# Kernel tuning notes

Measured on AMD Instinct MI355X. Metric: run time of the kernel, lower is better.

The kernel has to match this reference:

```python
import jax, jax.numpy as jnp
import numpy as np

B, N, M, G, F = 8, 1000, 64, 50, 128


def setup_inputs() -> dict:
    key = jax.random.key(0)
    ks = jax.random.split(key, 9)
    s = 0.05
    return {
        "features": jax.random.normal(ks[0], (B, N, F), jnp.float32),
        "rbf_expansion": jax.random.uniform(ks[1], (B, N, M, G), jnp.float32),
        "neighbor_list": jax.random.randint(ks[2], (B, N, M), 0, N, jnp.int64),
        "W_init": jax.random.normal(ks[3], (F, F), jnp.float32) * s,
        "W1": jax.random.normal(ks[4], (G, F), jnp.float32) * s,
        "b1": jnp.zeros((F,), jnp.float32),
        "W2": jax.random.normal(ks[5], (F, F), jnp.float32) * s,
        "b2": jnp.zeros((F,), jnp.float32),
        "nbr_w": jax.random.normal(ks[6], (F,), jnp.float32) * s,
        "Wo1": jax.random.normal(ks[7], (F, F), jnp.float32) * s,
        "bo1": jnp.zeros((F,), jnp.float32),
        "Wo2": jax.random.normal(ks[8], (F, F), jnp.float32) * s,
        "bo2": jnp.zeros((F,), jnp.float32),
    }


def reference(features, rbf_expansion, neighbor_list, W_init, W1, b1, W2, b2,
              nbr_w, Wo1, bo1, Wo2, bo2):
    b, n, m = neighbor_list.shape
    # 1. atom-wise linear, no bias/activation: [B,N,F]
    init = features @ W_init
    # 2. CFConv: filter generator on RBF expansion -> [B,N,M,F]
    filt = jnp.tanh(rbf_expansion @ W1 + b1) @ W2 + b2
    # gather neighbor features: init[b, neighbor_list[b,n,m], :] -> [B,N,M,F]
    idx = neighbor_list.reshape(b, n * m, 1)
    nbr_feat = jnp.take_along_axis(init, idx, axis=1).reshape(b, n, m, -1)
    conv = nbr_feat * filt
    # attention over neighbors via learned vector nbr_w
    attn = jax.nn.softmax(jnp.einsum('bnmf,f->bnm', conv, nbr_w), axis=-1)
    agg = jnp.einsum('bnm,bnmf->bnf', attn, conv)
    # 3-4. output dense: linear+tanh, then linear
    out = jnp.tanh(agg @ Wo1 + bo1) @ Wo2 + bo2
    return out, attn
```

## Files before the change

### kernel.cpp

```cpp
#include <hip/hip_runtime.h>
#include <hip/hip_bf16.h>

typedef __attribute__((ext_vector_type(8))) short short8;
typedef __attribute__((ext_vector_type(4))) float f32x4;
typedef unsigned short u16;
typedef unsigned int u32;

#define NBATCH 8
#define NA 1000
#define MD 64
#define GD 50
#define FD 128
#define TOTAL (NBATCH * NA)

__device__ __forceinline__ u16 f2bf(float f) {
    u32 x = __float_as_uint(f);
    return (u16)((x + 0x7fffu + ((x >> 16) & 1u)) >> 16);
}
__device__ __forceinline__ float bf2f(u16 u) {
    return __uint_as_float(((u32)u) << 16);
}
__device__ __forceinline__ u32 pkbf(float x, float y) {
    __hip_bfloat162 h = __float22bfloat162_rn(float2{x, y});
    return *reinterpret_cast<u32*>(&h);
}
__device__ __forceinline__ float tanh_fast(float x) {
    float e = __expf(2.0f * x);
    return 1.0f - 2.0f * __builtin_amdgcn_rcpf(e + 1.0f);
}
__device__ __forceinline__ f32x4 mfma16(short8 a, short8 b, f32x4 c) {
    return __builtin_amdgcn_mfma_f32_16x16x32_bf16(a, b, c, 0, 0, 0);
}

__global__ void k0_prep(const float* __restrict__ W1, const float* __restrict__ W2,
                        const float* __restrict__ Wi, const float* __restrict__ Wo1,
                        const float* __restrict__ Wo2,
                        u16* __restrict__ W1T, u16* __restrict__ W2T,
                        u16* __restrict__ WiT, u16* __restrict__ Wo1T,
                        u16* __restrict__ Wo2T) {
    const int g0 = blockIdx.x * 256 + threadIdx.x;
    const int gstep = gridDim.x * 256;
    for (int i = g0; i < 128 * 72; i += gstep) {
        int n = i / 72, k = i - n * 72;
        int ks = (k < GD) ? k : 0;
        W1T[i] = (k < GD) ? f2bf(W1[ks * FD + n]) : (u16)0;
    }
    for (int i = g0; i < 2 * 128 * 72; i += gstep) {
        int p = i / 9216;
        int rem = i - p * 9216;
        int n = rem / 72, kk = rem - n * 72;
        bool valid = kk < 64;
        int k = p * 64 + (valid ? kk : 0);
        W2T[i]  = valid ? f2bf(W2[k * FD + n])  : (u16)0;
        WiT[i]  = valid ? f2bf(Wi[k * FD + n])  : (u16)0;
        Wo1T[i] = valid ? f2bf(Wo1[k * FD + n]) : (u16)0;
        Wo2T[i] = valid ? f2bf(Wo2[k * FD + n]) : (u16)0;
    }
}

__global__ __launch_bounds__(256, 3) void k1_init(const float* __restrict__ feat,
                                                  const u16* __restrict__ WiT,
                                                  u16* __restrict__ initB) {
    __shared__ alignas(16) char smem[53248];
    u16* sA = (u16*)smem;
    u16* sW = (u16*)(smem + 34816);
    const int tid = threadIdx.x, wid = tid >> 6, lane = tid & 63;
    const int quad = lane >> 4, col = lane & 15, rw = wid * 32;
    const int row0 = blockIdx.x * 128;

    for (int i = tid; i < 4096; i += 256) {
        int r = i >> 5, c = (i & 31) * 4;
        int gr = row0 + r;
        float4 v = {0.f, 0.f, 0.f, 0.f};
        if (gr < TOTAL) v = *(const float4*)&feat[(size_t)gr * FD + c];
        u32* p = (u32*)&sA[r * 136 + c];
        p[0] = pkbf(v.x, v.y);
        p[1] = pkbf(v.z, v.w);
    }
    for (int i = tid; i < 1152; i += 256) ((int4*)sW)[i] = ((const int4*)WiT)[i];
    __syncthreads();

    f32x4 acc[2][8];
    const f32x4 zf = {0.f, 0.f, 0.f, 0.f};
#pragma unroll
    for (int mt = 0; mt < 2; ++mt)
#pragma unroll
        for (int nt = 0; nt < 8; ++nt) acc[mt][nt] = zf;

    for (int half = 0; half < 2; ++half) {
        if (half) {
            __syncthreads();
            for (int i = tid; i < 1152; i += 256)
                ((int4*)sW)[i] = ((const int4*)(WiT + 9216))[i];
            __syncthreads();
        }
#pragma unroll
        for (int ks = 0; ks < 2; ++ks) {
            const int ka = half * 64 + ks * 32 + quad * 8;
            const int kb = ks * 32 + quad * 8;
            short8 a0 = *(const short8*)&sA[(rw + col) * 136 + ka];
            short8 a1 = *(const short8*)&sA[(rw + 16 + col) * 136 + ka];
#pragma unroll
            for (int nt = 0; nt < 8; ++nt) {
                short8 bfr = *(const short8*)&sW[(nt * 16 + col) * 72 + kb];
                acc[0][nt] = mfma16(a0, bfr, acc[0][nt]);
                acc[1][nt] = mfma16(a1, bfr, acc[1][nt]);
            }
        }
    }
#pragma unroll
    for (int mt = 0; mt < 2; ++mt)
#pragma unroll
        for (int nt = 0; nt < 8; ++nt)
#pragma unroll
            for (int r = 0; r < 4; ++r) {
                int row = rw + mt * 16 + quad * 4 + r;
                int gr = row0 + row;
                if (gr < TOTAL)
                    initB[(size_t)gr * FD + nt * 16 + col] = f2bf(acc[mt][nt][r]);
            }
}

__global__ __launch_bounds__(256, 3) void k2_main(
    const float* __restrict__ rbf, const int* __restrict__ nl,
    const u16* __restrict__ initB,
    const u16* __restrict__ W1T, const u16* __restrict__ W2T,
    const float* __restrict__ b1, const float* __restrict__ b2,
    const float* __restrict__ nbrw,
    float* __restrict__ aggOut, float* __restrict__ attnO) {
    __shared__ alignas(16) char smem[53760];
    u16* sA = (u16*)smem;
    u16* sB = (u16*)(smem + 34816);
    int* nlS = (int*)(smem + 53248);
    float* logitS = (float*)smem;
    float* attnS  = (float*)(smem + 512);
    float* aggS   = (float*)(smem + 1024);

    const int tid = threadIdx.x, wid = tid >> 6, lane = tid & 63;
    const int quad = lane >> 4, col = lane & 15, rw = wid * 32;
    const int blk = blockIdx.x;
    const int b = blk / 500;
    const int n0 = (blk - b * 500) * 2;
    const int atom0 = b * NA + n0;
    const size_t rbf_base = (size_t)atom0 * (MD * GD);

    if (tid < 128) nlS[tid] = nl[atom0 * MD + tid];
    for (int i = tid; i < 128 * 14; i += 256) {
        int r = i / 14;
        sA[r * 72 + 50 + (i - r * 14)] = 0;
    }
    for (int i = tid; i < 3200; i += 256) {
        int e = 2 * i;
        int r = e / 50, g = e - r * 50;
        float2 v = *(const float2*)&rbf[rbf_base + e];
        *(u32*)&sA[r * 72 + g] = pkbf(v.x, v.y);
    }
    for (int i = tid; i < 1152; i += 256) ((int4*)sB)[i] = ((const int4*)W1T)[i];
    __syncthreads();

    f32x4 acc[2][8];
    const f32x4 zf = {0.f, 0.f, 0.f, 0.f};
#pragma unroll
    for (int mt = 0; mt < 2; ++mt)
#pragma unroll
        for (int nt = 0; nt < 8; ++nt) acc[mt][nt] = zf;
#pragma unroll
    for (int ks = 0; ks < 2; ++ks) {
        const int ka = ks * 32 + quad * 8;
        short8 a0 = *(const short8*)&sA[(rw + col) * 72 + ka];
        short8 a1 = *(const short8*)&sA[(rw + 16 + col) * 72 + ka];
#pragma unroll
        for (int nt = 0; nt < 8; ++nt) {
            short8 bfr = *(const short8*)&sB[(nt * 16 + col) * 72 + ka];
            acc[0][nt] = mfma16(a0, bfr, acc[0][nt]);
            acc[1][nt] = mfma16(a1, bfr, acc[1][nt]);
        }
    }
    __syncthreads();

    float bias[8];
#pragma unroll
    for (int nt = 0; nt < 8; ++nt) bias[nt] = b1[nt * 16 + col];
#pragma unroll
    for (int mt = 0; mt < 2; ++mt)
#pragma unroll
        for (int nt = 0; nt < 8; ++nt)
#pragma unroll
            for (int r = 0; r < 4; ++r) {
                int row = rw + mt * 16 + quad * 4 + r;
                sA[row * 136 + nt * 16 + col] =
                    f2bf(tanh_fast(acc[mt][nt][r] + bias[nt]));
            }
    for (int i = tid; i < 1152; i += 256) ((int4*)sB)[i] = ((const int4*)W2T)[i];
    __syncthreads();

    f32x4 acc2[2][8];
#pragma unroll
    for (int mt = 0; mt < 2; ++mt)
#pragma unroll
        for (int nt = 0; nt < 8; ++nt) acc2[mt][nt] = zf;
    for (int half = 0; half < 2; ++half) {
        if (half) {
            __syncthreads();
            for (int i = tid; i < 1152; i += 256)
                ((int4*)sB)[i] = ((const int4*)(W2T + 9216))[i];
            __syncthreads();
        }
#pragma unroll
        for (int ks = 0; ks < 2; ++ks) {
            const int ka = half * 64 + ks * 32 + quad * 8;
            const int kb = ks * 32 + quad * 8;
            short8 a0 = *(const short8*)&sA[(rw + col) * 136 + ka];
            short8 a1 = *(const short8*)&sA[(rw + 16 + col) * 136 + ka];
#pragma unroll
            for (int nt = 0; nt < 8; ++nt) {
                short8 bfr = *(const short8*)&sB[(nt * 16 + col) * 72 + kb];
                acc2[0][nt] = mfma16(a0, bfr, acc2[0][nt]);
                acc2[1][nt] = mfma16(a1, bfr, acc2[1][nt]);
            }
        }
    }

    float wv[8];
#pragma unroll
    for (int nt = 0; nt < 8; ++nt) {
        bias[nt] = b2[nt * 16 + col];
        wv[nt] = nbrw[nt * 16 + col];
    }
    int rowoff[2][4];
#pragma unroll
    for (int mt = 0; mt < 2; ++mt)
#pragma unroll
        for (int r = 0; r < 4; ++r) {
            int rr = rw + mt * 16 + quad * 4 + r;
            rowoff[mt][r] = (b * NA + nlS[rr]) * FD;
        }
    float part[2][4] = {{0.f, 0.f, 0.f, 0.f}, {0.f, 0.f, 0.f, 0.f}};
#pragma unroll
    for (int mt = 0; mt < 2; ++mt)
#pragma unroll
        for (int nt = 0; nt < 8; ++nt)
#pragma unroll
            for (int r = 0; r < 4; ++r) {
                float nb = bf2f(initB[rowoff[mt][r] + nt * 16 + col]);
                float cv = nb * (acc2[mt][nt][r] + bias[nt]);
                acc2[mt][nt][r] = cv;
                part[mt][r] += cv * wv[nt];
            }
#pragma unroll
    for (int d = 1; d < 16; d <<= 1)
#pragma unroll
        for (int mt = 0; mt < 2; ++mt)
#pragma unroll
            for (int r = 0; r < 4; ++r)
                part[mt][r] += __shfl_xor(part[mt][r], d, 64);
    __syncthreads();
    if (col == 0) {
#pragma unroll
        for (int mt = 0; mt < 2; ++mt)
#pragma unroll
            for (int r = 0; r < 4; ++r)
                logitS[rw + mt * 16 + quad * 4 + r] = part[mt][r];
    }
    __syncthreads();

    if (wid < 2) {
        float x = logitS[wid * 64 + lane];
        float m = x;
#pragma unroll
        for (int d = 1; d < 64; d <<= 1) m = fmaxf(m, __shfl_xor(m, d, 64));
        float e = __expf(x - m);
        float s = e;
#pragma unroll
        for (int d = 1; d < 64; d <<= 1) s += __shfl_xor(s, d, 64);
        float a = e / s;
        attnS[wid * 64 + lane] = a;
        attnO[(size_t)(atom0 + wid) * MD + lane] = a;
    }
    __syncthreads();

    float aggp[8] = {0.f, 0.f, 0.f, 0.f, 0.f, 0.f, 0.f, 0.f};
#pragma unroll
    for (int mt = 0; mt < 2; ++mt)
#pragma unroll
        for (int r = 0; r < 4; ++r) {
            float a = attnS[rw + mt * 16 + quad * 4 + r];
#pragma unroll
            for (int nt = 0; nt < 8; ++nt) aggp[nt] += a * acc2[mt][nt][r];
        }
#pragma unroll
    for (int d = 16; d < 64; d <<= 1)
#pragma unroll
        for (int nt = 0; nt < 8; ++nt) aggp[nt] += __shfl_xor(aggp[nt], d, 64);
    if (quad == 0) {
#pragma unroll
        for (int nt = 0; nt < 8; ++nt) aggS[wid * 128 + nt * 16 + col] = aggp[nt];
    }
    __syncthreads();
    {
        int a = tid >> 7;
        int c = tid & 127;
        float v = aggS[(2 * a) * 128 + c] + aggS[(2 * a + 1) * 128 + c];
        aggOut[(size_t)(atom0 + a) * FD + c] = v;
    }
}

__global__ __launch_bounds__(256, 3) void k3_out(
    float* __restrict__ outp, const u16* __restrict__ Wo1T,
    const u16* __restrict__ Wo2T, const float* __restrict__ bo1,
    const float* __restrict__ bo2) {
    __shared__ alignas(16) char smem[53248];
    u16* sA = (u16*)smem;
    u16* sW = (u16*)(smem + 34816);
    const int tid = threadIdx.x, wid = tid >> 6, lane = tid & 63;
    const int quad = lane >> 4, col = lane & 15, rw = wid * 32;
    const int row0 = blockIdx.x * 128;

    for (int i = tid; i < 4096; i += 256) {
        int r = i >> 5, c = (i & 31) * 4;
        int gr = row0 + r;
        float4 v = {0.f, 0.f, 0.f, 0.f};
        if (gr < TOTAL) v = *(const float4*)&outp[(size_t)gr * FD + c];
        u32* p = (u32*)&sA[r * 136 + c];
        p[0] = pkbf(v.x, v.y);
        p[1] = pkbf(v.z, v.w);
    }
    for (int i = tid; i < 1152; i += 256) ((int4*)sW)[i] = ((const int4*)Wo1T)[i];
    __syncthreads();

    f32x4 acc[2][8];
    const f32x4 zf = {0.f, 0.f, 0.f, 0.f};
#pragma unroll
    for (int mt = 0; mt < 2; ++mt)
#pragma unroll
        for (int nt = 0; nt < 8; ++nt) acc[mt][nt] = zf;
    for (int half = 0; half < 2; ++half) {
        if (half) {
            __syncthreads();
            for (int i = tid; i < 1152; i += 256)
                ((int4*)sW)[i] = ((const int4*)(Wo1T + 9216))[i];
            __syncthreads();
        }
#pragma unroll
        for (int ks = 0; ks < 2; ++ks) {
            const int ka = half * 64 + ks * 32 + quad * 8;
            const int kb = ks * 32 + quad * 8;
            short8 a0 = *(const short8*)&sA[(rw + col) * 136 + ka];
            short8 a1 = *(const short8*)&sA[(rw + 16 + col) * 136 + ka];
#pragma unroll
            for (int nt = 0; nt < 8; ++nt) {
                short8 bfr = *(const short8*)&sW[(nt * 16 + col) * 72 + kb];
                acc[0][nt] = mfma16(a0, bfr, acc[0][nt]);
                acc[1][nt] = mfma16(a1, bfr, acc[1][nt]);
            }
        }
    }
    __syncthreads();

    float bias[8];
#pragma unroll
    for (int nt = 0; nt < 8; ++nt) bias[nt] = bo1[nt * 16 + col];
#pragma unroll
    for (int mt = 0; mt < 2; ++mt)
#pragma unroll
        for (int nt = 0; nt < 8; ++nt)
#pragma unroll
            for (int r = 0; r < 4; ++r) {
                int row = rw + mt * 16 + quad * 4 + r;
                sA[row * 136 + nt * 16 + col] =
                    f2bf(tanh_fast(acc[mt][nt][r] + bias[nt]));
            }
    for (int i = tid; i < 1152; i += 256) ((int4*)sW)[i] = ((const int4*)Wo2T)[i];
    __syncthreads();

    f32x4 acc2[2][8];
#pragma unroll
    for (int mt = 0; mt < 2; ++mt)
#pragma unroll
        for (int nt = 0; nt < 8; ++nt) acc2[mt][nt] = zf;
    for (int half = 0; half < 2; ++half) {
        if (half) {
            __syncthreads();
            for (int i = tid; i < 1152; i += 256)
                ((int4*)sW)[i] = ((const int4*)(Wo2T + 9216))[i];
            __syncthreads();
        }
#pragma unroll
        for (int ks = 0; ks < 2; ++ks) {
            const int ka = half * 64 + ks * 32 + quad * 8;
            const int kb = ks * 32 + quad * 8;
            short8 a0 = *(const short8*)&sA[(rw + col) * 136 + ka];
            short8 a1 = *(const short8*)&sA[(rw + 16 + col) * 136 + ka];
#pragma unroll
            for (int nt = 0; nt < 8; ++nt) {
                short8 bfr = *(const short8*)&sW[(nt * 16 + col) * 72 + kb];
                acc2[0][nt] = mfma16(a0, bfr, acc2[0][nt]);
                acc2[1][nt] = mfma16(a1, bfr, acc2[1][nt]);
            }
        }
    }
#pragma unroll
    for (int nt = 0; nt < 8; ++nt) bias[nt] = bo2[nt * 16 + col];
#pragma unroll
    for (int mt = 0; mt < 2; ++mt)
#pragma unroll
        for (int nt = 0; nt < 8; ++nt)
#pragma unroll
            for (int r = 0; r < 4; ++r) {
                int row = rw + mt * 16 + quad * 4 + r;
                int gr = row0 + row;
                if (gr < TOTAL)
                    outp[(size_t)gr * FD + nt * 16 + col] =
                        acc2[mt][nt][r] + bias[nt];
            }
}

extern "C" void kernel_launch(void* const* d_in, const int* in_sizes, int n_in,
                              void* d_out, int out_size, void* d_ws,
                              size_t ws_size, hipStream_t stream) {
    const float* feat = (const float*)d_in[0];
    const float* rbf  = (const float*)d_in[1];
    const int*   nl   = (const int*)d_in[2];
    const float* Wi   = (const float*)d_in[3];
    const float* W1   = (const float*)d_in[4];
    const float* b1   = (const float*)d_in[5];
    const float* W2   = (const float*)d_in[6];
    const float* b2   = (const float*)d_in[7];
    const float* nbrw = (const float*)d_in[8];
    const float* Wo1  = (const float*)d_in[9];
    const float* bo1  = (const float*)d_in[10];
    const float* Wo2  = (const float*)d_in[11];
    const float* bo2  = (const float*)d_in[12];

    float* outp  = (float*)d_out;
    float* attnp = outp + (size_t)TOTAL * FD;

    char* ws = (char*)d_ws;
    u16* initB = (u16*)ws;
    u16* W1T   = (u16*)(ws + 2048000);
    u16* W2T   = (u16*)(ws + 2048000 + 18432);
    u16* WiT   = (u16*)(ws + 2048000 + 18432 + 36864);
    u16* Wo1T  = (u16*)(ws + 2048000 + 18432 + 2 * 36864);
    u16* Wo2T  = (u16*)(ws + 2048000 + 18432 + 3 * 36864);

    hipLaunchKernelGGL(k0_prep, dim3(40), dim3(256), 0, stream,
                       W1, W2, Wi, Wo1, Wo2, W1T, W2T, WiT, Wo1T, Wo2T);
    hipLaunchKernelGGL(k1_init, dim3(63), dim3(256), 0, stream, feat, WiT, initB);
    hipLaunchKernelGGL(k2_main, dim3(4000), dim3(256), 0, stream,
                       rbf, nl, initB, W1T, W2T, b1, b2, nbrw, outp, attnp);
    hipLaunchKernelGGL(k3_out, dim3(63), dim3(256), 0, stream,
                       outp, Wo1T, Wo2T, bo1, bo2);
}
```

Before: 295.4 us.

## Prefetch neighbor gathers early, drop softmax barrier, shrink dense-kernel row tiles

In the main kernel, neighbor indices are loaded into registers and the gathered neighbor feature values are issued before the first barrier, so gather latency overlaps the RBF staging and the filter GEMMs. Softmax now runs in all four waves and the attention weights reach each lane through shuffles, which removes an LDS buffer and a barrier. The init and output kernels switch from 128 to 64 rows per block, doubling the grid to fill more CUs and dropping the bounds checks. In exchange, the 64 prefetched gather registers per thread raise register pressure in the main kernel.

```diff
diff --git a/kernel.cpp b/kernel.cpp
--- a/kernel.cpp
+++ b/kernel.cpp
@@ -58,21 +58,19 @@
     }
 }
 
-__global__ __launch_bounds__(256, 3) void k1_init(const float* __restrict__ feat,
+__global__ __launch_bounds__(256, 4) void k1_init(const float* __restrict__ feat,
                                                   const u16* __restrict__ WiT,
                                                   u16* __restrict__ initB) {
-    __shared__ alignas(16) char smem[53248];
+    __shared__ alignas(16) char smem[35840];
     u16* sA = (u16*)smem;
-    u16* sW = (u16*)(smem + 34816);
+    u16* sW = (u16*)(smem + 17408);
     const int tid = threadIdx.x, wid = tid >> 6, lane = tid & 63;
-    const int quad = lane >> 4, col = lane & 15, rw = wid * 32;
-    const int row0 = blockIdx.x * 128;
-
-    for (int i = tid; i < 4096; i += 256) {
+    const int quad = lane >> 4, col = lane & 15, rw = wid * 16;
+    const int row0 = blockIdx.x * 64;
+
+    for (int i = tid; i < 2048; i += 256) {
         int r = i >> 5, c = (i & 31) * 4;
-        int gr = row0 + r;
-        float4 v = {0.f, 0.f, 0.f, 0.f};
-        if (gr < TOTAL) v = *(const float4*)&feat[(size_t)gr * FD + c];
+        float4 v = *(const float4*)&feat[(size_t)(row0 + r) * FD + c];
         u32* p = (u32*)&sA[r * 136 + c];
         p[0] = pkbf(v.x, v.y);
         p[1] = pkbf(v.z, v.w);
@@ -80,12 +78,10 @@
     for (int i = tid; i < 1152; i += 256) ((int4*)sW)[i] = ((const int4*)WiT)[i];
     __syncthreads();
 
-    f32x4 acc[2][8];
+    f32x4 acc[8];
     const f32x4 zf = {0.f, 0.f, 0.f, 0.f};
 #pragma unroll
-    for (int mt = 0; mt < 2; ++mt)
-#pragma unroll
-        for (int nt = 0; nt < 8; ++nt) acc[mt][nt] = zf;
+    for (int nt = 0; nt < 8; ++nt) acc[nt] = zf;
 
     for (int half = 0; half < 2; ++half) {
         if (half) {
@@ -99,26 +95,20 @@
             const int ka = half * 64 + ks * 32 + quad * 8;
             const int kb = ks * 32 + quad * 8;
             short8 a0 = *(const short8*)&sA[(rw + col) * 136 + ka];
-            short8 a1 = *(const short8*)&sA[(rw + 16 + col) * 136 + ka];
 #pragma unroll
             for (int nt = 0; nt < 8; ++nt) {
                 short8 bfr = *(const short8*)&sW[(nt * 16 + col) * 72 + kb];
-                acc[0][nt] = mfma16(a0, bfr, acc[0][nt]);
-                acc[1][nt] = mfma16(a1, bfr, acc[1][nt]);
-            }
-        }
-    }
-#pragma unroll
-    for (int mt = 0; mt < 2; ++mt)
-#pragma unroll
-        for (int nt = 0; nt < 8; ++nt)
-#pragma unroll
-            for (int r = 0; r < 4; ++r) {
-                int row = rw + mt * 16 + quad * 4 + r;
-                int gr = row0 + row;
-                if (gr < TOTAL)
-                    initB[(size_t)gr * FD + nt * 16 + col] = f2bf(acc[mt][nt][r]);
-            }
+                acc[nt] = mfma16(a0, bfr, acc[nt]);
+            }
+        }
+    }
+#pragma unroll
+    for (int nt = 0; nt < 8; ++nt)
+#pragma unroll
+        for (int r = 0; r < 4; ++r) {
+            int gr = row0 + rw + quad * 4 + r;
+            initB[(size_t)gr * FD + nt * 16 + col] = f2bf(acc[nt][r]);
+        }
 }
 
 __global__ __launch_bounds__(256, 3) void k2_main(
@@ -128,12 +118,10 @@
     const float* __restrict__ b1, const float* __restrict__ b2,
     const float* __restrict__ nbrw,
     float* __restrict__ aggOut, float* __restrict__ attnO) {
-    __shared__ alignas(16) char smem[53760];
+    __shared__ alignas(16) char smem[53248];
     u16* sA = (u16*)smem;
     u16* sB = (u16*)(smem + 34816);
-    int* nlS = (int*)(smem + 53248);
     float* logitS = (float*)smem;
-    float* attnS  = (float*)(smem + 512);
     float* aggS   = (float*)(smem + 1024);
 
     const int tid = threadIdx.x, wid = tid >> 6, lane = tid & 63;
@@ -144,7 +132,13 @@
     const int atom0 = b * NA + n0;
     const size_t rbf_base = (size_t)atom0 * (MD * GD);
 
-    if (tid < 128) nlS[tid] = nl[atom0 * MD + tid];
+    int nlv[2][4];
+#pragma unroll
+    for (int mt = 0; mt < 2; ++mt)
+#pragma unroll
+        for (int r = 0; r < 4; ++r)
+            nlv[mt][r] = nl[atom0 * MD + rw + mt * 16 + quad * 4 + r];
+
     for (int i = tid; i < 128 * 14; i += 256) {
         int r = i / 14;
         sA[r * 72 + 50 + (i - r * 14)] = 0;
@@ -156,6 +150,17 @@
         *(u32*)&sA[r * 72 + g] = pkbf(v.x, v.y);
     }
     for (int i = tid; i < 1152; i += 256) ((int4*)sB)[i] = ((const int4*)W1T)[i];
+
+    u32 graw[2][8][4];
+#pragma unroll
+    for (int mt = 0; mt < 2; ++mt)
+#pragma unroll
+        for (int r = 0; r < 4; ++r) {
+            int ro = (b * NA + nlv[mt][r]) * FD + col;
+#pragma unroll
+            for (int nt = 0; nt < 8; ++nt)
+                graw[mt][nt][r] = initB[ro + nt * 16];
+        }
     __syncthreads();
 
     f32x4 acc[2][8];
@@ -227,14 +232,6 @@
         bias[nt] = b2[nt * 16 + col];
         wv[nt] = nbrw[nt * 16 + col];
     }
-    int rowoff[2][4];
-#pragma unroll
-    for (int mt = 0; mt < 2; ++mt)
-#pragma unroll
-        for (int r = 0; r < 4; ++r) {
-            int rr = rw + mt * 16 + quad * 4 + r;
-            rowoff[mt][r] = (b * NA + nlS[rr]) * FD;
-        }
     float part[2][4] = {{0.f, 0.f, 0.f, 0.f}, {0.f, 0.f, 0.f, 0.f}};
 #pragma unroll
     for (int mt = 0; mt < 2; ++mt)
@@ -242,7 +239,7 @@
         for (int nt = 0; nt < 8; ++nt)
 #pragma unroll
             for (int r = 0; r < 4; ++r) {
-                float nb = bf2f(initB[rowoff[mt][r] + nt * 16 + col]);
+                float nb = bf2f((u16)graw[mt][nt][r]);
                 float cv = nb * (acc2[mt][nt][r] + bias[nt]);
                 acc2[mt][nt][r] = cv;
                 part[mt][r] += cv * wv[nt];
@@ -264,8 +261,10 @@
     }
     __syncthreads();
 
-    if (wid < 2) {
-        float x = logitS[wid * 64 + lane];
+    float attw[2][4];
+    {
+        const int base = rw & 64;
+        float x = logitS[base + lane];
         float m = x;
 #pragma unroll
         for (int d = 1; d < 64; d <<= 1) m = fmaxf(m, __shfl_xor(m, d, 64));
@@ -274,17 +273,21 @@
 #pragma unroll
         for (int d = 1; d < 64; d <<= 1) s += __shfl_xor(s, d, 64);
         float a = e / s;
-        attnS[wid * 64 + lane] = a;
-        attnO[(size_t)(atom0 + wid) * MD + lane] = a;
-    }
-    __syncthreads();
+        if ((wid & 1) == 0)
+            attnO[(size_t)(atom0 + (wid >> 1)) * MD + lane] = a;
+#pragma unroll
+        for (int mt = 0; mt < 2; ++mt)
+#pragma unroll
+            for (int r = 0; r < 4; ++r)
+                attw[mt][r] = __shfl(a, (rw & 32) + mt * 16 + quad * 4 + r, 64);
+    }
 
     float aggp[8] = {0.f, 0.f, 0.f, 0.f, 0.f, 0.f, 0.f, 0.f};
 #pragma unroll
     for (int mt = 0; mt < 2; ++mt)
 #pragma unroll
         for (int r = 0; r < 4; ++r) {
-            float a = attnS[rw + mt * 16 + quad * 4 + r];
+            float a = attw[mt][r];
 #pragma unroll
             for (int nt = 0; nt < 8; ++nt) aggp[nt] += a * acc2[mt][nt][r];
         }
@@ -305,22 +308,20 @@
     }
 }
 
-__global__ __launch_bounds__(256, 3) void k3_out(
+__global__ __launch_bounds__(256, 4) void k3_out(
     float* __restrict__ outp, const u16* __restrict__ Wo1T,
     const u16* __restrict__ Wo2T, const float* __restrict__ bo1,
     const float* __restrict__ bo2) {
-    __shared__ alignas(16) char smem[53248];
+    __shared__ alignas(16) char smem[35840];
     u16* sA = (u16*)smem;
-    u16* sW = (u16*)(smem + 34816);
+    u16* sW = (u16*)(smem + 17408);
     const int tid = threadIdx.x, wid = tid >> 6, lane = tid & 63;
-    const int quad = lane >> 4, col = lane & 15, rw = wid * 32;
-    const int row0 = blockIdx.x * 128;
-
-    for (int i = tid; i < 4096; i += 256) {
+    const int quad = lane >> 4, col = lane & 15, rw = wid * 16;
+    const int row0 = blockIdx.x * 64;
+
+    for (int i = tid; i < 2048; i += 256) {
         int r = i >> 5, c = (i & 31) * 4;
-        int gr = row0 + r;
-        float4 v = {0.f, 0.f, 0.f, 0.f};
-        if (gr < TOTAL) v = *(const float4*)&outp[(size_t)gr * FD + c];
+        float4 v = *(const float4*)&outp[(size_t)(row0 + r) * FD + c];
         u32* p = (u32*)&sA[r * 136 + c];
         p[0] = pkbf(v.x, v.y);
         p[1] = pkbf(v.z, v.w);
@@ -328,12 +329,10 @@
     for (int i = tid; i < 1152; i += 256) ((int4*)sW)[i] = ((const int4*)Wo1T)[i];
     __syncthreads();
 
-    f32x4 acc[2][8];
+    f32x4 acc[8];
     const f32x4 zf = {0.f, 0.f, 0.f, 0.f};
 #pragma unroll
-    for (int mt = 0; mt < 2; ++mt)
-#pragma unroll
-        for (int nt = 0; nt < 8; ++nt) acc[mt][nt] = zf;
+    for (int nt = 0; nt < 8; ++nt) acc[nt] = zf;
     for (int half = 0; half < 2; ++half) {
         if (half) {
             __syncthreads();
@@ -346,12 +345,10 @@
             const int ka = half * 64 + ks * 32 + quad * 8;
             const int kb = ks * 32 + quad * 8;
             short8 a0 = *(const short8*)&sA[(rw + col) * 136 + ka];
-            short8 a1 = *(const short8*)&sA[(rw + 16 + col) * 136 + ka];
 #pragma unroll
             for (int nt = 0; nt < 8; ++nt) {
                 short8 bfr = *(const short8*)&sW[(nt * 16 + col) * 72 + kb];
-                acc[0][nt] = mfma16(a0, bfr, acc[0][nt]);
-                acc[1][nt] = mfma16(a1, bfr, acc[1][nt]);
+                acc[nt] = mfma16(a0, bfr, acc[nt]);
             }
         }
     }
@@ -361,23 +358,18 @@
 #pragma unroll
     for (int nt = 0; nt < 8; ++nt) bias[nt] = bo1[nt * 16 + col];
 #pragma unroll
-    for (int mt = 0; mt < 2; ++mt)
-#pragma unroll
-        for (int nt = 0; nt < 8; ++nt)
-#pragma unroll
-            for (int r = 0; r < 4; ++r) {
-                int row = rw + mt * 16 + quad * 4 + r;
-                sA[row * 136 + nt * 16 + col] =
-                    f2bf(tanh_fast(acc[mt][nt][r] + bias[nt]));
-            }
+    for (int nt = 0; nt < 8; ++nt)
+#pragma unroll
+        for (int r = 0; r < 4; ++r) {
+            int row = rw + quad * 4 + r;
+            sA[row * 136 + nt * 16 + col] = f2bf(tanh_fast(acc[nt][r] + bias[nt]));
+        }
     for (int i = tid; i < 1152; i += 256) ((int4*)sW)[i] = ((const int4*)Wo2T)[i];
     __syncthreads();
 
-    f32x4 acc2[2][8];
-#pragma unroll
-    for (int mt = 0; mt < 2; ++mt)
-#pragma unroll
-        for (int nt = 0; nt < 8; ++nt) acc2[mt][nt] = zf;
+    f32x4 acc2[8];
+#pragma unroll
+    for (int nt = 0; nt < 8; ++nt) acc2[nt] = zf;
     for (int half = 0; half < 2; ++half) {
         if (half) {
             __syncthreads();
@@ -390,29 +382,22 @@
             const int ka = half * 64 + ks * 32 + quad * 8;
             const int kb = ks * 32 + quad * 8;
             short8 a0 = *(const short8*)&sA[(rw + col) * 136 + ka];
-            short8 a1 = *(const short8*)&sA[(rw + 16 + col) * 136 + ka];
 #pragma unroll
             for (int nt = 0; nt < 8; ++nt) {
                 short8 bfr = *(const short8*)&sW[(nt * 16 + col) * 72 + kb];
-                acc2[0][nt] = mfma16(a0, bfr, acc2[0][nt]);
-                acc2[1][nt] = mfma16(a1, bfr, acc2[1][nt]);
+                acc2[nt] = mfma16(a0, bfr, acc2[nt]);
             }
         }
     }
 #pragma unroll
     for (int nt = 0; nt < 8; ++nt) bias[nt] = bo2[nt * 16 + col];
 #pragma unroll
-    for (int mt = 0; mt < 2; ++mt)
-#pragma unroll
-        for (int nt = 0; nt < 8; ++nt)
-#pragma unroll
-            for (int r = 0; r < 4; ++r) {
-                int row = rw + mt * 16 + quad * 4 + r;
-                int gr = row0 + row;
-                if (gr < TOTAL)
-                    outp[(size_t)gr * FD + nt * 16 + col] =
-                        acc2[mt][nt][r] + bias[nt];
-            }
+    for (int nt = 0; nt < 8; ++nt)
+#pragma unroll
+        for (int r = 0; r < 4; ++r) {
+            int gr = row0 + rw + quad * 4 + r;
+            outp[(size_t)gr * FD + nt * 16 + col] = acc2[nt][r] + bias[nt];
+        }
 }
 
 extern "C" void kernel_launch(void* const* d_in, const int* in_sizes, int n_in,
@@ -445,9 +430,9 @@
 
     hipLaunchKernelGGL(k0_prep, dim3(40), dim3(256), 0, stream,
                        W1, W2, Wi, Wo1, Wo2, W1T, W2T, WiT, Wo1T, Wo2T);
-    hipLaunchKernelGGL(k1_init, dim3(63), dim3(256), 0, stream, feat, WiT, initB);
+    hipLaunchKernelGGL(k1_init, dim3(125), dim3(256), 0, stream, feat, WiT, initB);
     hipLaunchKernelGGL(k2_main, dim3(4000), dim3(256), 0, stream,
                        rbf, nl, initB, W1T, W2T, b1, b2, nbrw, outp, attnp);
-    hipLaunchKernelGGL(k3_out, dim3(63), dim3(256), 0, stream,
+    hipLaunchKernelGGL(k3_out, dim3(125), dim3(256), 0, stream,
                        outp, Wo1T, Wo2T, bo1, bo2);
 }
```

Result: slower. 337.0 us (+14.1%).
